# Kernel tuning notes

Measured on AMD Instinct MI355X. Metric: run time of the kernel, lower is better.

The kernel has to match this reference:

```python
import jax, jax.numpy as jnp
import numpy as np

B, N, NBR, C = 1, 2048, 32, 384
C1, OUT = 32, 128


def setup_inputs() -> dict:
    key = jax.random.key(0)
    ks = jax.random.split(key, 6)
    return {
        "s_i": jax.random.normal(ks[0], (B, N, C), dtype=jnp.float32),
        "s_j": jax.random.normal(ks[1], (B, N, NBR, C), dtype=jnp.float32),
        "m_i": jnp.ones((B, N), dtype=jnp.float32),
        "m_j": jnp.ones((B, N, NBR), dtype=jnp.float32),
        "Wl": jax.random.normal(ks[2], (C, C1), dtype=jnp.float32) * (C ** -0.5),
        "bl": jnp.zeros((C1,), dtype=jnp.float32),
        "Wr": jax.random.normal(ks[3], (C, C1), dtype=jnp.float32) * (C ** -0.5),
        "br": jnp.zeros((C1,), dtype=jnp.float32),
        "Wo": jax.random.normal(ks[4], (C1 * C1, OUT), dtype=jnp.float32) * ((C1 * C1) ** -0.5),
        "bo": jnp.zeros((OUT,), dtype=jnp.float32),
    }


def reference(s_i, s_j, m_i, m_j, Wl, bl, Wr, br, Wo, bo):
    # Masked projections
    left = m_i[..., None] * (jnp.einsum('bic,ca->bia', s_i, Wl) + bl)      # (B, N, C1)
    right = m_j[..., None] * (jnp.einsum('bikc,ca->bika', s_j, Wr) + br)   # (B, N, n, C1)
    # Per-(residue, neighbor) outer product; equals the repeat/reshape/transpose
    # dance in the original: out[b,i,k,a*C1+c] = left[b,i,a] * right[b,i,k,c]
    op = jnp.einsum('bia,bikc->bikac', left, right)                        # (B, N, n, C1, C1)
    b_, n_, k_ = op.shape[:3]
    op = op.reshape(b_, n_, k_, C1 * C1)
    # Output projection
    return jnp.einsum('bikd,do->biko', op, Wo) + bo                        # (B, N, n, OUT)
```

## Files before the change

### kernel.cpp

```cpp
#include <hip/hip_runtime.h>

constexpr int NRES = 2048;
constexpr int NBR  = 32;
constexpr int C    = 384;
constexpr int C1   = 32;
constexpr int OUTD = 128;

__global__ __launch_bounds__(256, 6) void outerprod_kernel(
    const float* __restrict__ s_i, const float* __restrict__ s_j,
    const float* __restrict__ m_i, const float* __restrict__ m_j,
    const float* __restrict__ Wl,  const float* __restrict__ bl,
    const float* __restrict__ Wr,  const float* __restrict__ br,
    const float* __restrict__ Wo,  const float* __restrict__ bo,
    float* __restrict__ out)
{
    const int i = blockIdx.x;
    const int t = threadIdx.x;

    __shared__ float red[8][C1];
    __shared__ float lft[C1];
    __shared__ float rgt[NBR * C1];
    __shared__ float Tm[C1 * OUTD];

    {
        const int a = t & 31, g = t >> 5;
        const float* si = s_i + (size_t)i * C;
        const int c0 = g * 48;
        float acc = 0.f;
        #pragma unroll 4
        for (int c = c0; c < c0 + 48; c += 4) {
            const float4 s4 = *reinterpret_cast<const float4*>(si + c);
            acc = fmaf(s4.x, Wl[(c + 0) * C1 + a], acc);
            acc = fmaf(s4.y, Wl[(c + 1) * C1 + a], acc);
            acc = fmaf(s4.z, Wl[(c + 2) * C1 + a], acc);
            acc = fmaf(s4.w, Wl[(c + 3) * C1 + a], acc);
        }
        red[g][a] = acc;
    }
    __syncthreads();

    if (t < C1) {
        float acc = bl[t];
        #pragma unroll
        for (int g = 0; g < 8; ++g) acc += red[g][t];
        lft[t] = m_i[i] * acc;
    }

    {
        const int k = t >> 3, cg = t & 7;
        const float* sr = s_j + ((size_t)i * NBR + k) * C;
        const float* wr = Wr + cg * 4;
        float a0 = 0.f, a1 = 0.f, a2 = 0.f, a3 = 0.f;
        #pragma unroll 4
        for (int cc = 0; cc < C; cc += 4) {
            const float4 s4 = *reinterpret_cast<const float4*>(sr + cc);
            float4 w;
            w = *reinterpret_cast<const float4*>(wr + (cc + 0) * C1);
            a0 = fmaf(s4.x, w.x, a0); a1 = fmaf(s4.x, w.y, a1);
            a2 = fmaf(s4.x, w.z, a2); a3 = fmaf(s4.x, w.w, a3);
            w = *reinterpret_cast<const float4*>(wr + (cc + 1) * C1);
            a0 = fmaf(s4.y, w.x, a0); a1 = fmaf(s4.y, w.y, a1);
            a2 = fmaf(s4.y, w.z, a2); a3 = fmaf(s4.y, w.w, a3);
            w = *reinterpret_cast<const float4*>(wr + (cc + 2) * C1);
            a0 = fmaf(s4.z, w.x, a0); a1 = fmaf(s4.z, w.y, a1);
            a2 = fmaf(s4.z, w.z, a2); a3 = fmaf(s4.z, w.w, a3);
            w = *reinterpret_cast<const float4*>(wr + (cc + 3) * C1);
            a0 = fmaf(s4.w, w.x, a0); a1 = fmaf(s4.w, w.y, a1);
            a2 = fmaf(s4.w, w.z, a2); a3 = fmaf(s4.w, w.w, a3);
        }
        const float  m  = m_j[i * NBR + k];
        const float4 b4 = *reinterpret_cast<const float4*>(br + cg * 4);
        rgt[k * C1 + cg * 4 + 0] = m * (a0 + b4.x);
        rgt[k * C1 + cg * 4 + 1] = m * (a1 + b4.y);
        rgt[k * C1 + cg * 4 + 2] = m * (a2 + b4.z);
        rgt[k * C1 + cg * 4 + 3] = m * (a3 + b4.w);
    }
    __syncthreads();

    #pragma unroll
    for (int j = 0; j < 4; ++j) {
        const int e4 = t + j * 256;
        const int c  = e4 >> 5;
        const int o  = (e4 & 31) * 4;
        float a0 = 0.f, a1 = 0.f, a2 = 0.f, a3 = 0.f;
        #pragma unroll 8
        for (int a = 0; a < C1; ++a) {
            const float  l  = lft[a];
            const float4 w4 = *reinterpret_cast<const float4*>(
                Wo + ((size_t)(a * C1 + c)) * OUTD + o);
            a0 = fmaf(l, w4.x, a0); a1 = fmaf(l, w4.y, a1);
            a2 = fmaf(l, w4.z, a2); a3 = fmaf(l, w4.w, a3);
        }
        float4 r = {a0, a1, a2, a3};
        *reinterpret_cast<float4*>(&Tm[c * OUTD + o]) = r;
    }
    __syncthreads();

    #pragma unroll
    for (int j = 0; j < 4; ++j) {
        const int e4 = t + j * 256;
        const int k  = e4 >> 5;
        const int o  = (e4 & 31) * 4;
        const float4 b4 = *reinterpret_cast<const float4*>(bo + o);
        float a0 = b4.x, a1 = b4.y, a2 = b4.z, a3 = b4.w;
        #pragma unroll 8
        for (int c = 0; c < C1; ++c) {
            const float  r  = rgt[k * C1 + c];
            const float4 tv = *reinterpret_cast<const float4*>(&Tm[c * OUTD + o]);
            a0 = fmaf(r, tv.x, a0); a1 = fmaf(r, tv.y, a1);
            a2 = fmaf(r, tv.z, a2); a3 = fmaf(r, tv.w, a3);
        }
        const float4 res = {a0, a1, a2, a3};
        *reinterpret_cast<float4*>(&out[((size_t)i * NBR + k) * OUTD + o]) = res;
    }
}

extern "C" void kernel_launch(void* const* d_in, const int* in_sizes, int n_in,
                              void* d_out, int out_size, void* d_ws, size_t ws_size,
                              hipStream_t stream) {
    (void)in_sizes; (void)n_in; (void)out_size; (void)d_ws; (void)ws_size;
    const float* s_i = (const float*)d_in[0];
    const float* s_j = (const float*)d_in[1];
    const float* m_i = (const float*)d_in[2];
    const float* m_j = (const float*)d_in[3];
    const float* Wl  = (const float*)d_in[4];
    const float* bl  = (const float*)d_in[5];
    const float* Wr  = (const float*)d_in[6];
    const float* br  = (const float*)d_in[7];
    const float* Wo  = (const float*)d_in[8];
    const float* bo  = (const float*)d_in[9];
    float* out = (float*)d_out;

    outerprod_kernel<<<NRES, 256, 0, stream>>>(
        s_i, s_j, m_i, m_j, Wl, bl, Wr, br, Wo, bo, out);
}
```

Measured before the change: 325.6 us.

## Stage s_j rows through double-buffered shared memory with coalesced prefetch

The s_j projection used to read s_j straight from global memory, with the 8 threads of each neighbour row reading the same float4, which gives strided, redundant accesses. It now loads 64-column chunks of all 32 neighbour rows into padded, double-buffered shared memory, using coalesced float4 loads. The next chunk is prefetched into registers while the current one is computed. This adds about 17 KB of LDS and a barrier per chunk, and lowers the launch-bounds occupancy hint from 6 to 4 blocks per SM.

New measurement: 317.9 us. 1.02x faster.

```diff
diff --git a/kernel.cpp b/kernel.cpp
--- a/kernel.cpp
+++ b/kernel.cpp
@@ -6,7 +6,11 @@
 constexpr int C1   = 32;
 constexpr int OUTD = 128;
 
-__global__ __launch_bounds__(256, 6) void outerprod_kernel(
+constexpr int CHUNK = 64;
+constexpr int NCH   = C / CHUNK;
+constexpr int SJ_LD = CHUNK + 4;
+
+__global__ __launch_bounds__(256, 4) void outerprod_kernel(
     const float* __restrict__ s_i, const float* __restrict__ s_j,
     const float* __restrict__ m_i, const float* __restrict__ m_j,
     const float* __restrict__ Wl,  const float* __restrict__ bl,
@@ -21,6 +25,14 @@
     __shared__ float lft[C1];
     __shared__ float rgt[NBR * C1];
     __shared__ float Tm[C1 * OUTD];
+    __shared__ float sj[2][NBR * SJ_LD];
+
+    const int f0 = t,        kk0 = f0 >> 4, c40 = (f0 & 15) * 4;
+    const int f1 = t + 256,  kk1 = f1 >> 4, c41 = (f1 & 15) * 4;
+    const float* sjbase = s_j + (size_t)i * NBR * C;
+
+    float4 st0 = *reinterpret_cast<const float4*>(sjbase + kk0 * C + c40);
+    float4 st1 = *reinterpret_cast<const float4*>(sjbase + kk1 * C + c41);
 
     {
         const int a = t & 31, g = t >> 5;
@@ -39,6 +51,9 @@
     }
     __syncthreads();
 
+    *reinterpret_cast<float4*>(&sj[0][kk0 * SJ_LD + c40]) = st0;
+    *reinterpret_cast<float4*>(&sj[0][kk1 * SJ_LD + c41]) = st1;
+
     if (t < C1) {
         float acc = bl[t];
         #pragma unroll
@@ -46,34 +61,49 @@
         lft[t] = m_i[i] * acc;
     }
 
+    const int k = t >> 3, cg = t & 7;
+    float acc0 = 0.f, acc1 = 0.f, acc2 = 0.f, acc3 = 0.f;
+    int cur = 0;
+    for (int ch = 0; ch < NCH; ++ch) {
+        if (ch + 1 < NCH) {
+            st0 = *reinterpret_cast<const float4*>(sjbase + kk0 * C + (ch + 1) * CHUNK + c40);
+            st1 = *reinterpret_cast<const float4*>(sjbase + kk1 * C + (ch + 1) * CHUNK + c41);
+        }
+        __syncthreads();
+
+        const float* srow  = &sj[cur][k * SJ_LD];
+        const float* wbase = Wr + (size_t)(ch * CHUNK) * C1 + cg * 4;
+        #pragma unroll
+        for (int c4 = 0; c4 < CHUNK / 4; ++c4) {
+            const float4 s4 = *reinterpret_cast<const float4*>(srow + c4 * 4);
+            float4 w;
+            w = *reinterpret_cast<const float4*>(wbase + (c4 * 4 + 0) * C1);
+            acc0 = fmaf(s4.x, w.x, acc0); acc1 = fmaf(s4.x, w.y, acc1);
+            acc2 = fmaf(s4.x, w.z, acc2); acc3 = fmaf(s4.x, w.w, acc3);
+            w = *reinterpret_cast<const float4*>(wbase + (c4 * 4 + 1) * C1);
+            acc0 = fmaf(s4.y, w.x, acc0); acc1 = fmaf(s4.y, w.y, acc1);
+            acc2 = fmaf(s4.y, w.z, acc2); acc3 = fmaf(s4.y, w.w, acc3);
+            w = *reinterpret_cast<const float4*>(wbase + (c4 * 4 + 2) * C1);
+            acc0 = fmaf(s4.z, w.x, acc0); acc1 = fmaf(s4.z, w.y, acc1);
+            acc2 = fmaf(s4.z, w.z, acc2); acc3 = fmaf(s4.z, w.w, acc3);
+            w = *reinterpret_cast<const float4*>(wbase + (c4 * 4 + 3) * C1);
+            acc0 = fmaf(s4.w, w.x, acc0); acc1 = fmaf(s4.w, w.y, acc1);
+            acc2 = fmaf(s4.w, w.z, acc2); acc3 = fmaf(s4.w, w.w, acc3);
+        }
+
+        if (ch + 1 < NCH) {
+            *reinterpret_cast<float4*>(&sj[cur ^ 1][kk0 * SJ_LD + c40]) = st0;
+            *reinterpret_cast<float4*>(&sj[cur ^ 1][kk1 * SJ_LD + c41]) = st1;
+        }
+        cur ^= 1;
+    }
     {
-        const int k = t >> 3, cg = t & 7;
-        const float* sr = s_j + ((size_t)i * NBR + k) * C;
-        const float* wr = Wr + cg * 4;
-        float a0 = 0.f, a1 = 0.f, a2 = 0.f, a3 = 0.f;
-        #pragma unroll 4
-        for (int cc = 0; cc < C; cc += 4) {
-            const float4 s4 = *reinterpret_cast<const float4*>(sr + cc);
-            float4 w;
-            w = *reinterpret_cast<const float4*>(wr + (cc + 0) * C1);
-            a0 = fmaf(s4.x, w.x, a0); a1 = fmaf(s4.x, w.y, a1);
-            a2 = fmaf(s4.x, w.z, a2); a3 = fmaf(s4.x, w.w, a3);
-            w = *reinterpret_cast<const float4*>(wr + (cc + 1) * C1);
-            a0 = fmaf(s4.y, w.x, a0); a1 = fmaf(s4.y, w.y, a1);
-            a2 = fmaf(s4.y, w.z, a2); a3 = fmaf(s4.y, w.w, a3);
-            w = *reinterpret_cast<const float4*>(wr + (cc + 2) * C1);
-            a0 = fmaf(s4.z, w.x, a0); a1 = fmaf(s4.z, w.y, a1);
-            a2 = fmaf(s4.z, w.z, a2); a3 = fmaf(s4.z, w.w, a3);
-            w = *reinterpret_cast<const float4*>(wr + (cc + 3) * C1);
-            a0 = fmaf(s4.w, w.x, a0); a1 = fmaf(s4.w, w.y, a1);
-            a2 = fmaf(s4.w, w.z, a2); a3 = fmaf(s4.w, w.w, a3);
-        }
         const float  m  = m_j[i * NBR + k];
         const float4 b4 = *reinterpret_cast<const float4*>(br + cg * 4);
-        rgt[k * C1 + cg * 4 + 0] = m * (a0 + b4.x);
-        rgt[k * C1 + cg * 4 + 1] = m * (a1 + b4.y);
-        rgt[k * C1 + cg * 4 + 2] = m * (a2 + b4.z);
-        rgt[k * C1 + cg * 4 + 3] = m * (a3 + b4.w);
+        rgt[k * C1 + cg * 4 + 0] = m * (acc0 + b4.x);
+        rgt[k * C1 + cg * 4 + 1] = m * (acc1 + b4.y);
+        rgt[k * C1 + cg * 4 + 2] = m * (acc2 + b4.z);
+        rgt[k * C1 + cg * 4 + 3] = m * (acc3 + b4.w);
     }
     __syncthreads();
 
@@ -99,19 +129,19 @@
     #pragma unroll
     for (int j = 0; j < 4; ++j) {
         const int e4 = t + j * 256;
-        const int k  = e4 >> 5;
+        const int kk = e4 >> 5;
         const int o  = (e4 & 31) * 4;
         const float4 b4 = *reinterpret_cast<const float4*>(bo + o);
         float a0 = b4.x, a1 = b4.y, a2 = b4.z, a3 = b4.w;
         #pragma unroll 8
         for (int c = 0; c < C1; ++c) {
-            const float  r  = rgt[k * C1 + c];
+            const float  r  = rgt[kk * C1 + c];
             const float4 tv = *reinterpret_cast<const float4*>(&Tm[c * OUTD + o]);
             a0 = fmaf(r, tv.x, a0); a1 = fmaf(r, tv.y, a1);
             a2 = fmaf(r, tv.z, a2); a3 = fmaf(r, tv.w, a3);
         }
         const float4 res = {a0, a1, a2, a3};
-        *reinterpret_cast<float4*>(&out[((size_t)i * NBR + k) * OUTD + o]) = res;
+        *reinterpret_cast<float4*>(&out[((size_t)i * NBR + kk) * OUTD + o]) = res;
     }
 }
 
```
